# Kernel tuning notes

Measured on AMD Instinct MI355X. Metric: run time of the kernel, lower is better.

The kernel has to match this reference:

```python
import jax, jax.numpy as jnp
import numpy as np

D = 768
H = 12
DH = D // H


def setup_inputs() -> dict:
    key = jax.random.key(0)
    ks = jax.random.split(key, 7)
    B, S = 8, 1024
    sequences = jax.random.normal(ks[0], (B, S, D), dtype=jnp.float32)
    # per-head Linear params: weight [H, DH, DH] (torch Linear convention y = x W^T + b), bias [H, DH]
    scale = 1.0 / np.sqrt(DH)
    Wq = jax.random.uniform(ks[1], (H, DH, DH), jnp.float32, -scale, scale)
    Wk = jax.random.uniform(ks[2], (H, DH, DH), jnp.float32, -scale, scale)
    Wv = jax.random.uniform(ks[3], (H, DH, DH), jnp.float32, -scale, scale)
    bq = jax.random.uniform(ks[4], (H, DH), jnp.float32, -scale, scale)
    bk = jax.random.uniform(ks[5], (H, DH), jnp.float32, -scale, scale)
    bv = jax.random.uniform(ks[6], (H, DH), jnp.float32, -scale, scale)
    return {"sequences": sequences, "Wq": Wq, "Wk": Wk, "Wv": Wv,
            "bq": bq, "bk": bk, "bv": bv}


def reference(sequences, Wq, Wk, Wv, bq, bk, bv):
    B, S, _ = sequences.shape
    x = sequences.reshape(B, S, H, DH)  # head slices along feature dim
    # torch Linear: y = x @ W.T + b  ->  einsum over last dim of W
    Q = jnp.einsum('bshd,hed->bshe', x, Wq) + bq
    K = jnp.einsum('bshd,hed->bshe', x, Wk) + bk
    V = jnp.einsum('bshd,hed->bshe', x, Wv) + bv
    scores = jnp.einsum('bshe,bthe->bhst', Q, K) / np.sqrt(DH).astype(np.float32)
    attn = jax.nn.softmax(scores, axis=-1)  # [B,H,S,S]
    out = jnp.einsum('bhst,bthd->bshd', attn, V)
    return out.reshape(B, S, H * DH)
```

## Files before the change

### kernel.cpp

```cpp
#include <hip/hip_runtime.h>

#define NH 12
#define DHEAD 64
#define DMODEL 768
#define SEQ 1024
#define NBH 96

typedef _Float16 h8 __attribute__((ext_vector_type(8)));
typedef _Float16 h4 __attribute__((ext_vector_type(4)));
typedef __fp16   fp16x2 __attribute__((ext_vector_type(2)));
typedef float f32x4 __attribute__((ext_vector_type(4)));


__global__ __launch_bounds__(256) void proj_kernel(
    const float* __restrict__ x,
    const float* __restrict__ Wq, const float* __restrict__ Wk,
    const float* __restrict__ Wv,
    const float* __restrict__ bq, const float* __restrict__ bk,
    const float* __restrict__ bv,
    _Float16* __restrict__ Qf, _Float16* __restrict__ Kf,
    _Float16* __restrict__ Vf)
{
    __shared__ _Float16 xh[128][72];
    __shared__ _Float16 yh[128][72];

    const int h    = blockIdx.y;
    const int mtx  = blockIdx.z;
    const int tid  = threadIdx.x;
    const int row0 = blockIdx.x * 128;
    const int lane = tid & 63;
    const int w    = tid >> 6;
    const int g    = lane >> 4;
    const int r    = lane & 15;

    const int b    = row0 >> 10;
    const int bh   = b * NH + h;
    const int s16b = (row0 & 1023) >> 4;
    const int s32b = (row0 & 1023) >> 5;

#pragma unroll
    for (int p = 0; p < 8; ++p) {
        const int rr = p * 16 + (tid >> 4);
        const int c4 = (tid & 15) * 4;
        float4 v = *(const float4*)(x + (size_t)(row0 + rr) * DMODEL
                                      + h * DHEAD + c4);
        h4 o = { (_Float16)v.x, (_Float16)v.y, (_Float16)v.z, (_Float16)v.w };
        *(h4*)(&xh[rr][c4]) = o;
    }

    const float* W    = (mtx == 0 ? Wq : (mtx == 1 ? Wk : Wv)) + h * DHEAD * DHEAD;
    const float* bias = (mtx == 0 ? bq : (mtx == 1 ? bk : bv)) + h * DHEAD;
    const float  ws   = (mtx == 0) ? 0.125f * 1.44269504f : 1.0f;

    h8 bf[4][2];
    float bcol[4];
#pragma unroll
    for (int n = 0; n < 4; ++n) {
        const float* Wr = W + (n * 16 + r) * DHEAD;
#pragma unroll
        for (int hf = 0; hf < 2; ++hf) {
            const float* p = Wr + hf * 32 + g * 8;
            float4 w0 = *(const float4*)(p);
            float4 w1 = *(const float4*)(p + 4);
            h8 o = { (_Float16)(w0.x * ws), (_Float16)(w0.y * ws),
                     (_Float16)(w0.z * ws), (_Float16)(w0.w * ws),
                     (_Float16)(w1.x * ws), (_Float16)(w1.y * ws),
                     (_Float16)(w1.z * ws), (_Float16)(w1.w * ws) };
            bf[n][hf] = o;
        }
        bcol[n] = bias[n * 16 + r] * ws;
    }
    __syncthreads();

#pragma unroll
    for (int gg = 0; gg < 2; ++gg) {
        const int gi = w + gg * 4;
        const h8 af0 = *(const h8*)(&xh[gi * 16 + r][g * 8]);
        const h8 af1 = *(const h8*)(&xh[gi * 16 + r][32 + g * 8]);
#pragma unroll
        for (int n = 0; n < 4; ++n) {
            f32x4 d = { bcol[n], bcol[n], bcol[n], bcol[n] };
            d = __builtin_amdgcn_mfma_f32_16x16x32_f16(af0, bf[n][0], d, 0, 0, 0);
            d = __builtin_amdgcn_mfma_f32_16x16x32_f16(af1, bf[n][1], d, 0, 0, 0);
#pragma unroll
            for (int reg = 0; reg < 4; ++reg)
                yh[gi * 16 + g * 4 + reg][n * 16 + r] = (_Float16)d[reg];
        }
    }
    __syncthreads();

    if (mtx < 2) {
        const int s16l = tid >> 5;
        const int lx   = tid & 31;
        h8* dstb = (h8*)(mtx == 0 ? Qf : Kf)
                 + ((size_t)(bh * 64 + s16b + s16l)) * 128;
#pragma unroll
        for (int hf = 0; hf < 2; ++hf)
#pragma unroll
            for (int li = 0; li < 2; ++li) {
                const int ln  = lx + li * 32;
                const int gg2 = ln >> 4, rr2 = ln & 15;
                h8 v = *(const h8*)(&yh[s16l * 16 + rr2][hf * 32 + gg2 * 8]);
                dstb[hf * 64 + ln] = v;
            }
    } else {
        const int s32l = tid >> 6;
        const int t    = (tid >> 4) & 3;
        const int li   = tid & 15;
        h8 wv[4];
#pragma unroll
        for (int k = 0; k < 4; ++k) {
            const int ln  = li * 4 + k;
            const int gg2 = ln >> 4, rr2 = ln & 15;
#pragma unroll
            for (int j = 0; j < 4; ++j) {
                wv[k][j]     = yh[s32l * 32 +      gg2 * 4 + j][t * 16 + rr2];
                wv[k][j + 4] = yh[s32l * 32 + 16 + gg2 * 4 + j][t * 16 + rr2];
            }
        }
        h8* dst = (h8*)Vf
                + (((size_t)(bh * 32 + s32b + s32l)) * 4 + t) * 64 + li * 4;
#pragma unroll
        for (int k = 0; k < 4; ++k) dst[k] = wv[k];
    }
}

__global__ __launch_bounds__(256, 4) void attn_kernel(
    const _Float16* __restrict__ Qf, const _Float16* __restrict__ Kf,
    const _Float16* __restrict__ Vf, float* __restrict__ out)
{
    __shared__ _Float16 kbuf[2][2048];
    __shared__ _Float16 vbuf[2][2048];

    const int orig    = blockIdx.x;
    const int logical = (orig & 7) * 96 + (orig >> 3);
    const int bh      = logical >> 3;
    const int qblk    = logical & 7;
    const int tid  = threadIdx.x;
    const int lane = tid & 63;
    const int w    = tid >> 6;
    const int g    = lane >> 4;
    const int r    = lane & 15;

    const h8* Qb = (const h8*)Qf + (size_t)bh * 64 * 128;
    const h8* Kb = (const h8*)Kf + (size_t)bh * 64 * 128;
    const h8* Vb = (const h8*)Vf + (size_t)bh * 32 * 256;

    const int q16_0 = qblk * 8 + w * 2;

    h8 qf[2][2];
#pragma unroll
    for (int qg = 0; qg < 2; ++qg) {
        qf[qg][0] = Qb[(q16_0 + qg) * 128 + lane];
        qf[qg][1] = Qb[(q16_0 + qg) * 128 + 64 + lane];
    }

    f32x4 ot[2][4] = {};
    float lsum[2] = {};

#define STAGE(c, buf)                                                         \
    {                                                                         \
        const h8* gk = Kb + (size_t)(c) * 256 + w * 64 + lane;                \
        const h8* gv = Vb + (size_t)(c) * 256 + w * 64 + lane;                \
        __builtin_amdgcn_global_load_lds(                                     \
            (const __attribute__((address_space(1))) void*)gk,                \
            (__attribute__((address_space(3))) void*)(&kbuf[buf][w * 512]),   \
            16, 0, 0);                                                        \
        __builtin_amdgcn_global_load_lds(                                     \
            (const __attribute__((address_space(1))) void*)gv,                \
            (__attribute__((address_space(3))) void*)(&vbuf[buf][w * 512]),   \
            16, 0, 0);                                                        \
    }

    STAGE(0, 0)
    __syncthreads();

#pragma unroll 2
    for (int c = 0; c < 32; ++c) {
        const int cur = c & 1;
        if (c < 31) STAGE(c + 1, cur ^ 1)

        __builtin_amdgcn_s_setprio(1);
        h8 kr0[2], kr1[2];
        kr0[0] = *(const h8*)(&kbuf[cur][0 * 512 + lane * 8]);
        kr0[1] = *(const h8*)(&kbuf[cur][1 * 512 + lane * 8]);
        kr1[0] = *(const h8*)(&kbuf[cur][2 * 512 + lane * 8]);
        kr1[1] = *(const h8*)(&kbuf[cur][3 * 512 + lane * 8]);

        f32x4 s[2][2];
#pragma unroll
        for (int qg = 0; qg < 2; ++qg) {
            s[qg][0] = __builtin_amdgcn_mfma_f32_16x16x32_f16(
                kr0[0], qf[qg][0], (f32x4){0.f, 0.f, 0.f, 0.f}, 0, 0, 0);
            s[qg][0] = __builtin_amdgcn_mfma_f32_16x16x32_f16(
                kr0[1], qf[qg][1], s[qg][0], 0, 0, 0);
            s[qg][1] = __builtin_amdgcn_mfma_f32_16x16x32_f16(
                kr1[0], qf[qg][0], (f32x4){0.f, 0.f, 0.f, 0.f}, 0, 0, 0);
            s[qg][1] = __builtin_amdgcn_mfma_f32_16x16x32_f16(
                kr1[1], qf[qg][1], s[qg][1], 0, 0, 0);
        }

        h8 up[2];
#pragma unroll
        for (int qg = 0; qg < 2; ++qg) {
            float p0 = __builtin_amdgcn_exp2f(s[qg][0][0]);
            float p1 = __builtin_amdgcn_exp2f(s[qg][0][1]);
            float p2 = __builtin_amdgcn_exp2f(s[qg][0][2]);
            float p3 = __builtin_amdgcn_exp2f(s[qg][0][3]);
            float p4 = __builtin_amdgcn_exp2f(s[qg][1][0]);
            float p5 = __builtin_amdgcn_exp2f(s[qg][1][1]);
            float p6 = __builtin_amdgcn_exp2f(s[qg][1][2]);
            float p7 = __builtin_amdgcn_exp2f(s[qg][1][3]);
            lsum[qg] += ((p0 + p1) + (p2 + p3)) + ((p4 + p5) + (p6 + p7));
            union { fp16x2 v2[4]; h8 v8; } u;
            u.v2[0] = __builtin_amdgcn_cvt_pkrtz(p0, p1);
            u.v2[1] = __builtin_amdgcn_cvt_pkrtz(p2, p3);
            u.v2[2] = __builtin_amdgcn_cvt_pkrtz(p4, p5);
            u.v2[3] = __builtin_amdgcn_cvt_pkrtz(p6, p7);
            up[qg] = u.v8;
        }

#pragma unroll
        for (int t = 0; t < 4; ++t) {
            h8 vr = *(const h8*)(&vbuf[cur][t * 512 + lane * 8]);
            ot[0][t] = __builtin_amdgcn_mfma_f32_16x16x32_f16(
                vr, up[0], ot[0][t], 0, 0, 0);
            ot[1][t] = __builtin_amdgcn_mfma_f32_16x16x32_f16(
                vr, up[1], ot[1][t], 0, 0, 0);
        }
        __builtin_amdgcn_s_setprio(0);

        __syncthreads();
    }
#undef STAGE

    const int b = bh / NH, h = bh % NH;
#pragma unroll
    for (int qg = 0; qg < 2; ++qg) {
        float l = lsum[qg];
        l += __shfl_xor(l, 16);
        l += __shfl_xor(l, 32);
        const float inv = 1.0f / l;
        float* op = out + ((size_t)b * SEQ + (q16_0 + qg) * 16 + r) * DMODEL
                  + h * DHEAD + g * 4;
#pragma unroll
        for (int t = 0; t < 4; ++t) {
            float4 res = { ot[qg][t][0] * inv, ot[qg][t][1] * inv,
                           ot[qg][t][2] * inv, ot[qg][t][3] * inv };
            *(float4*)(op + t * 16) = res;
        }
    }
}

extern "C" void kernel_launch(void* const* d_in, const int* in_sizes, int n_in,
                              void* d_out, int out_size, void* d_ws, size_t ws_size,
                              hipStream_t stream)
{
    const float* x  = (const float*)d_in[0];
    const float* Wq = (const float*)d_in[1];
    const float* Wk = (const float*)d_in[2];
    const float* Wv = (const float*)d_in[3];
    const float* bq = (const float*)d_in[4];
    const float* bk = (const float*)d_in[5];
    const float* bv = (const float*)d_in[6];
    float* out = (float*)d_out;

    const size_t frag_elems = (size_t)NBH * 64 * 2 * 64 * 8;
    _Float16* Qf = (_Float16*)d_ws;
    _Float16* Kf = Qf + frag_elems;
    _Float16* Vf = Kf + frag_elems;

    proj_kernel<<<dim3(64, 12, 3), 256, 0, stream>>>(x, Wq, Wk, Wv, bq, bk, bv,
                                                     Qf, Kf, Vf);
    attn_kernel<<<768, 256, 0, stream>>>(Qf, Kf, Vf, out);
}
```

Before: 63.96 us.

## Deepen attention K/V pipeline to four LDS buffers with one barrier per chunk

```diff
diff --git a/kernel.cpp b/kernel.cpp
--- a/kernel.cpp
+++ b/kernel.cpp
@@ -129,8 +129,8 @@
     const _Float16* __restrict__ Qf, const _Float16* __restrict__ Kf,
     const _Float16* __restrict__ Vf, float* __restrict__ out)
 {
-    __shared__ _Float16 kbuf[2][2048];
-    __shared__ _Float16 vbuf[2][2048];
+    __shared__ _Float16 kbuf[4][2048];
+    __shared__ _Float16 vbuf[4][2048];
 
     const int orig    = blockIdx.x;
     const int logical = (orig & 7) * 96 + (orig >> 3);
@@ -154,6 +154,7 @@
         qf[qg][0] = Qb[(q16_0 + qg) * 128 + lane];
         qf[qg][1] = Qb[(q16_0 + qg) * 128 + 64 + lane];
     }
+    asm volatile("s_waitcnt vmcnt(0)" ::: "memory");
 
     f32x4 ot[2][4] = {};
     float lsum[2] = {};
@@ -172,66 +173,72 @@
             16, 0, 0);                                                        \
     }
 
+#define CHUNK(c, VM, DOSTAGE)                                                 \
+    {                                                                         \
+        if (DOSTAGE) STAGE((c) + 2, ((c) + 2) & 3)                            \
+        asm volatile("s_waitcnt vmcnt(" #VM ")" ::: "memory");                \
+        __builtin_amdgcn_s_barrier();                                         \
+        const int cur = (c) & 3;                                              \
+        __builtin_amdgcn_s_setprio(1);                                        \
+        h8 kr0[2], kr1[2];                                                    \
+        kr0[0] = *(const h8*)(&kbuf[cur][0 * 512 + lane * 8]);                \
+        kr0[1] = *(const h8*)(&kbuf[cur][1 * 512 + lane * 8]);                \
+        kr1[0] = *(const h8*)(&kbuf[cur][2 * 512 + lane * 8]);                \
+        kr1[1] = *(const h8*)(&kbuf[cur][3 * 512 + lane * 8]);                \
+        f32x4 s[2][2];                                                        \
+        _Pragma("unroll")                                                     \
+        for (int qg = 0; qg < 2; ++qg) {                                      \
+            s[qg][0] = __builtin_amdgcn_mfma_f32_16x16x32_f16(                \
+                kr0[0], qf[qg][0], (f32x4){0.f, 0.f, 0.f, 0.f}, 0, 0, 0);     \
+            s[qg][0] = __builtin_amdgcn_mfma_f32_16x16x32_f16(                \
+                kr0[1], qf[qg][1], s[qg][0], 0, 0, 0);                        \
+            s[qg][1] = __builtin_amdgcn_mfma_f32_16x16x32_f16(                \
+                kr1[0], qf[qg][0], (f32x4){0.f, 0.f, 0.f, 0.f}, 0, 0, 0);     \
+            s[qg][1] = __builtin_amdgcn_mfma_f32_16x16x32_f16(                \
+                kr1[1], qf[qg][1], s[qg][1], 0, 0, 0);                        \
+        }                                                                     \
+        h8 up[2];                                                             \
+        _Pragma("unroll")                                                     \
+        for (int qg = 0; qg < 2; ++qg) {                                      \
+            float p0 = __builtin_amdgcn_exp2f(s[qg][0][0]);                   \
+            float p1 = __builtin_amdgcn_exp2f(s[qg][0][1]);                   \
+            float p2 = __builtin_amdgcn_exp2f(s[qg][0][2]);                   \
+            float p3 = __builtin_amdgcn_exp2f(s[qg][0][3]);                   \
+            float p4 = __builtin_amdgcn_exp2f(s[qg][1][0]);                   \
+            float p5 = __builtin_amdgcn_exp2f(s[qg][1][1]);                   \
+            float p6 = __builtin_amdgcn_exp2f(s[qg][1][2]);                   \
+            float p7 = __builtin_amdgcn_exp2f(s[qg][1][3]);                   \
+            lsum[qg] += ((p0 + p1) + (p2 + p3)) + ((p4 + p5) + (p6 + p7));    \
+            union { fp16x2 v2[4]; h8 v8; } u;                                 \
+            u.v2[0] = __builtin_amdgcn_cvt_pkrtz(p0, p1);                     \
+            u.v2[1] = __builtin_amdgcn_cvt_pkrtz(p2, p3);                     \
+            u.v2[2] = __builtin_amdgcn_cvt_pkrtz(p4, p5);                     \
+            u.v2[3] = __builtin_amdgcn_cvt_pkrtz(p6, p7);                     \
+            up[qg] = u.v8;                                                    \
+        }                                                                     \
+        _Pragma("unroll")                                                     \
+        for (int t = 0; t < 4; ++t) {                                         \
+            h8 vr = *(const h8*)(&vbuf[cur][t * 512 + lane * 8]);             \
+            ot[0][t] = __builtin_amdgcn_mfma_f32_16x16x32_f16(                \
+                vr, up[0], ot[0][t], 0, 0, 0);                                \
+            ot[1][t] = __builtin_amdgcn_mfma_f32_16x16x32_f16(                \
+                vr, up[1], ot[1][t], 0, 0, 0);                                \
+        }                                                                     \
+        __builtin_amdgcn_s_setprio(0);                                        \
+    }
+
     STAGE(0, 0)
-    __syncthreads();
-
-#pragma unroll 2
-    for (int c = 0; c < 32; ++c) {
-        const int cur = c & 1;
-        if (c < 31) STAGE(c + 1, cur ^ 1)
-
-        __builtin_amdgcn_s_setprio(1);
-        h8 kr0[2], kr1[2];
-        kr0[0] = *(const h8*)(&kbuf[cur][0 * 512 + lane * 8]);
-        kr0[1] = *(const h8*)(&kbuf[cur][1 * 512 + lane * 8]);
-        kr1[0] = *(const h8*)(&kbuf[cur][2 * 512 + lane * 8]);
-        kr1[1] = *(const h8*)(&kbuf[cur][3 * 512 + lane * 8]);
-
-        f32x4 s[2][2];
-#pragma unroll
-        for (int qg = 0; qg < 2; ++qg) {
-            s[qg][0] = __builtin_amdgcn_mfma_f32_16x16x32_f16(
-                kr0[0], qf[qg][0], (f32x4){0.f, 0.f, 0.f, 0.f}, 0, 0, 0);
-            s[qg][0] = __builtin_amdgcn_mfma_f32_16x16x32_f16(
-                kr0[1], qf[qg][1], s[qg][0], 0, 0, 0);
-            s[qg][1] = __builtin_amdgcn_mfma_f32_16x16x32_f16(
-                kr1[0], qf[qg][0], (f32x4){0.f, 0.f, 0.f, 0.f}, 0, 0, 0);
-            s[qg][1] = __builtin_amdgcn_mfma_f32_16x16x32_f16(
-                kr1[1], qf[qg][1], s[qg][1], 0, 0, 0);
-        }
-
-        h8 up[2];
-#pragma unroll
-        for (int qg = 0; qg < 2; ++qg) {
-            float p0 = __builtin_amdgcn_exp2f(s[qg][0][0]);
-            float p1 = __builtin_amdgcn_exp2f(s[qg][0][1]);
-            float p2 = __builtin_amdgcn_exp2f(s[qg][0][2]);
-            float p3 = __builtin_amdgcn_exp2f(s[qg][0][3]);
-            float p4 = __builtin_amdgcn_exp2f(s[qg][1][0]);
-            float p5 = __builtin_amdgcn_exp2f(s[qg][1][1]);
-            float p6 = __builtin_amdgcn_exp2f(s[qg][1][2]);
-            float p7 = __builtin_amdgcn_exp2f(s[qg][1][3]);
-            lsum[qg] += ((p0 + p1) + (p2 + p3)) + ((p4 + p5) + (p6 + p7));
-            union { fp16x2 v2[4]; h8 v8; } u;
-            u.v2[0] = __builtin_amdgcn_cvt_pkrtz(p0, p1);
-            u.v2[1] = __builtin_amdgcn_cvt_pkrtz(p2, p3);
-            u.v2[2] = __builtin_amdgcn_cvt_pkrtz(p4, p5);
-            u.v2[3] = __builtin_amdgcn_cvt_pkrtz(p6, p7);
-            up[qg] = u.v8;
-        }
-
-#pragma unroll
-        for (int t = 0; t < 4; ++t) {
-            h8 vr = *(const h8*)(&vbuf[cur][t * 512 + lane * 8]);
-            ot[0][t] = __builtin_amdgcn_mfma_f32_16x16x32_f16(
-                vr, up[0], ot[0][t], 0, 0, 0);
-            ot[1][t] = __builtin_amdgcn_mfma_f32_16x16x32_f16(
-                vr, up[1], ot[1][t], 0, 0, 0);
-        }
-        __builtin_amdgcn_s_setprio(0);
-
-        __syncthreads();
-    }
+    STAGE(1, 1)
+
+    CHUNK(0, 4, 1)  CHUNK(1, 4, 1)  CHUNK(2, 4, 1)  CHUNK(3, 4, 1)
+    CHUNK(4, 4, 1)  CHUNK(5, 4, 1)  CHUNK(6, 4, 1)  CHUNK(7, 4, 1)
+    CHUNK(8, 4, 1)  CHUNK(9, 4, 1)  CHUNK(10, 4, 1) CHUNK(11, 4, 1)
+    CHUNK(12, 4, 1) CHUNK(13, 4, 1) CHUNK(14, 4, 1) CHUNK(15, 4, 1)
+    CHUNK(16, 4, 1) CHUNK(17, 4, 1) CHUNK(18, 4, 1) CHUNK(19, 4, 1)
+    CHUNK(20, 4, 1) CHUNK(21, 4, 1) CHUNK(22, 4, 1) CHUNK(23, 4, 1)
+    CHUNK(24, 4, 1) CHUNK(25, 4, 1) CHUNK(26, 4, 1) CHUNK(27, 4, 1)
+    CHUNK(28, 4, 1) CHUNK(29, 4, 1) CHUNK(30, 2, 0) CHUNK(31, 0, 0)
+#undef CHUNK
 #undef STAGE
 
     const int b = bh / NH, h = bh % NH;
```

Result: no change. 65.19 us (+1.9%).
